# Optimization experiments

Hardware: AMD Instinct MI355X
Metric: run time of the kernel (lower is better)

The kernel has to match this reference:

```python
import jax, jax.numpy as jnp
import numpy as np

NUM_CATEGORIES = 32
INPUT_DIM = 1536
HIDDEN_DIM = 1024
OUTPUT_DIM = 1024
B, T = 128, 32


def setup_inputs() -> dict:
    key = jax.random.key(0)
    k_x, k_cat, k_w1, k_w2 = jax.random.split(key, 4)
    x = jax.random.normal(k_x, (B, T, INPUT_DIM), dtype=jnp.float32)
    cat_ids = jax.random.randint(k_cat, (B,), 0, NUM_CATEGORIES)
    # CategorySpecificLinear params: W ~ 0.02*randn, b = zeros
    W1 = 0.02 * jax.random.normal(k_w1, (NUM_CATEGORIES, INPUT_DIM, HIDDEN_DIM), dtype=jnp.float32)
    b1 = jnp.zeros((NUM_CATEGORIES, HIDDEN_DIM), dtype=jnp.float32)
    W2 = 0.02 * jax.random.normal(k_w2, (NUM_CATEGORIES, HIDDEN_DIM, OUTPUT_DIM), dtype=jnp.float32)
    b2 = jnp.zeros((NUM_CATEGORIES, OUTPUT_DIM), dtype=jnp.float32)
    return {"x": x, "cat_ids": cat_ids, "W1": W1, "b1": b1, "W2": W2, "b2": b2}


def _cat_linear(x, W, b, cat_ids):
    # x: (B, T, D_in); W: (C, D_in, D_out); b: (C, D_out)
    # torch: bmm(x, W[cat_ids]) + b[cat_ids].unsqueeze(1)
    return jnp.einsum("btd,bdh->bth", x, W[cat_ids]) + b[cat_ids][:, None, :]


def reference(x, cat_ids, W1, b1, W2, b2):
    # CategorySpecificMLP.forward
    hidden = jax.nn.relu(_cat_linear(x, W1, b1, cat_ids))  # (B, T, H)
    return _cat_linear(hidden, W2, b2, cat_ids)            # (B, T, O)
```

## Files before the change

kernel.cpp:

```cpp
#include <hip/hip_runtime.h>
#include <hip/hip_bf16.h>
#include <stdint.h>

#define NCAT 32
#define DIN  1536
#define DMID 1024
#define NB   128
#define TT   32

#define BM 128
#define BN 64
#define BK 32
#define LDA 40
#define MAXG 56
#define NTILE 16

typedef __attribute__((ext_vector_type(8))) short short8;
typedef __attribute__((ext_vector_type(4))) float f32x4;

static __device__ __forceinline__ unsigned int pk2bf(float lo, float hi) {
  unsigned short a = __builtin_bit_cast(unsigned short, __float2bfloat16(lo));
  unsigned short b = __builtin_bit_cast(unsigned short, __float2bfloat16(hi));
  return ((unsigned int)b << 16) | (unsigned int)a;
}

__global__ void build_groups(const int* __restrict__ cat_ids, int* __restrict__ wsi) {
  __shared__ int cats[NB];
  __shared__ int cnt[NCAT];
  __shared__ int off[NCAT];
  int t = threadIdx.x;
  cats[t] = cat_ids[t];
  __syncthreads();
  if (t < NCAT) {
    int n = 0;
    for (int b = 0; b < NB; b++) n += (cats[b] == t);
    cnt[t] = n;
  }
  __syncthreads();
  if (t == 0) {
    int acc = 0;
    for (int c = 0; c < NCAT; c++) { off[c] = acc; acc += cnt[c]; }
  }
  __syncthreads();
  if (t < NCAT) {
    int o = off[t];
    for (int b = 0; b < NB; b++)
      if (cats[b] == t) wsi[o++] = b;
  }
  if (t == 0) {
    int g = 0;
    for (int c = 0; c < NCAT; c++) {
      int n = cnt[c], o = off[c];
      for (int j = 0; j < n; j += 4) {
        wsi[132 + g * 4 + 0] = c;
        wsi[132 + g * 4 + 1] = o + j;
        wsi[132 + g * 4 + 2] = (n - j) < 4 ? (n - j) : 4;
        g++;
      }
    }
    wsi[128] = g;
  }
}

__global__ void cvt_x_bf16(const float* __restrict__ in, unsigned short* __restrict__ out) {
  int i = blockIdx.x * 256 + threadIdx.x;
  const float4* p = (const float4*)in + (size_t)i * 2;
  float4 a = p[0], b = p[1];
  ((uint4*)out)[i] = make_uint4(pk2bf(a.x, a.y), pk2bf(a.z, a.w),
                                pk2bf(b.x, b.y), pk2bf(b.z, b.w));
}

template <int LAYER>
__global__ __launch_bounds__(256)
void mlp_gemm(const unsigned short* __restrict__ A, const float* __restrict__ W,
              const float* __restrict__ bias, const int* __restrict__ wsi,
              void* __restrict__ Out, int K) {
  const int id = blockIdx.x;
  const int g  = (id & 7) + 8 * (id >> 7);
  const int t  = (id >> 3) & 15;
  if (g >= wsi[128]) return;
  const int cat   = wsi[132 + g * 4 + 0];
  const int start = wsi[132 + g * 4 + 1];
  const int cnt   = wsi[132 + g * 4 + 2];
  const int n0    = t * BN;

  __shared__ unsigned short As[2][BM * LDA];
  __shared__ unsigned short Bs[2][4 * BN * 8];

  const int tid  = threadIdx.x;
  const int lane = tid & 63;
  const int w    = tid >> 6;

  const int arow  = tid >> 1;
  const int khalf = (tid & 1) * 16;
  const int lb    = arow >> 5;
  const int tok   = arow & 31;
  const int lbc   = lb < (cnt - 1) ? lb : (cnt - 1);
  const int batch = wsi[start + lbc];
  const long grow = (long)(batch * TT + tok);
  const unsigned short* Arow = A + grow * (long)K + khalf;

  const float* Wcol = W + (size_t)cat * (size_t)K * 1024 + n0 + lane;

  f32x4 acc[4][2];
#pragma unroll
  for (int i = 0; i < 4; i++)
#pragma unroll
    for (int j = 0; j < 2; j++) acc[i][j] = (f32x4){0.f, 0.f, 0.f, 0.f};

  const int wm  = (w >> 1) * 64;
  const int wn  = (w & 1) * 32;
  const int kg  = lane >> 4;
  const int c16 = lane & 15;

  uint4 a0, a1;
  float br[8];
  auto load_tile = [&](int k0) {
    const uint4* ap = (const uint4*)(Arow + k0);
    a0 = ap[0];
    a1 = ap[1];
    const float* bp = Wcol + (size_t)(k0 + w * 8) * 1024;
#pragma unroll
    for (int r = 0; r < 8; r++) br[r] = bp[(size_t)r * 1024];
  };
  auto store_tile = [&](int buf) {
    *(uint4*)&As[buf][arow * LDA + khalf]     = a0;
    *(uint4*)&As[buf][arow * LDA + khalf + 8] = a1;
    uint4 bw = make_uint4(pk2bf(br[0], br[1]), pk2bf(br[2], br[3]),
                          pk2bf(br[4], br[5]), pk2bf(br[6], br[7]));
    *(uint4*)&Bs[buf][(w * BN + lane) * 8] = bw;
  };

  load_tile(0);
  store_tile(0);
  int cur = 0;

  for (int k0 = 0; k0 < K; k0 += BK) {
    __syncthreads();
    const bool more = (k0 + BK) < K;
    if (more) load_tile(k0 + BK);

    short8 afrag[4], bfrag[2];
#pragma unroll
    for (int i = 0; i < 4; i++)
      afrag[i] = *(const short8*)&As[cur][(wm + i * 16 + c16) * LDA + kg * 8];
#pragma unroll
    for (int j = 0; j < 2; j++)
      bfrag[j] = *(const short8*)&Bs[cur][(kg * BN + wn + j * 16 + c16) * 8];
#pragma unroll
    for (int i = 0; i < 4; i++)
#pragma unroll
      for (int j = 0; j < 2; j++)
        acc[i][j] = __builtin_amdgcn_mfma_f32_16x16x32_bf16(afrag[i], bfrag[j], acc[i][j], 0, 0, 0);

    if (more) store_tile(cur ^ 1);
    cur ^= 1;
  }

  const int rquad = (lane >> 4) * 4;
#pragma unroll
  for (int i = 0; i < 4; i++) {
#pragma unroll
    for (int j = 0; j < 2; j++) {
      int gcol = n0 + wn + j * 16 + c16;
      float bb = bias[cat * 1024 + gcol];
#pragma unroll
      for (int r = 0; r < 4; r++) {
        int lrow = wm + i * 16 + rquad + r;
        int lb2 = lrow >> 5;
        if (lb2 < cnt) {
          int b2 = wsi[start + lb2];
          long orow = (long)(b2 * TT + (lrow & 31));
          float v = acc[i][j][r] + bb;
          if constexpr (LAYER == 1) {
            v = fmaxf(v, 0.f);
            ((unsigned short*)Out)[orow * DMID + gcol] =
                __builtin_bit_cast(unsigned short, __float2bfloat16(v));
          } else {
            ((float*)Out)[orow * 1024 + gcol] = v;
          }
        }
      }
    }
  }
}

extern "C" void kernel_launch(void* const* d_in, const int* in_sizes, int n_in,
                              void* d_out, int out_size, void* d_ws, size_t ws_size,
                              hipStream_t stream) {
  const float* x       = (const float*)d_in[0];
  const int*   cat_ids = (const int*)d_in[1];
  const float* W1      = (const float*)d_in[2];
  const float* b1      = (const float*)d_in[3];
  const float* W2      = (const float*)d_in[4];
  const float* b2      = (const float*)d_in[5];
  float* out = (float*)d_out;

  int* wsi = (int*)d_ws;
  unsigned short* xbf    = (unsigned short*)((char*)d_ws + 8192);
  unsigned short* hidden = (unsigned short*)((char*)d_ws + 8192 + 12582912);

  build_groups<<<dim3(1), dim3(128), 0, stream>>>(cat_ids, wsi);
  cvt_x_bf16<<<dim3(3072), dim3(256), 0, stream>>>(x, xbf);
  mlp_gemm<1><<<dim3(NTILE * MAXG), dim3(256), 0, stream>>>(
      xbf, W1, b1, wsi, (void*)hidden, DIN);
  mlp_gemm<2><<<dim3(NTILE * MAXG), dim3(256), 0, stream>>>(
      hidden, W2, b2, wsi, (void*)out, DMID);
}
```

Before: 446.7 us.

## Deepen global-load prefetch to four register stages with LDS-only barriers

Replaces the single-tile register prefetch with four rotating register stages, so global loads for A and W are issued three k-tiles ahead of their LDS store. The plain __syncthreads is replaced by a barrier that waits only on LDS counters, so outstanding global loads stay in flight across barriers. This aims to hide the latency of the strided fp32 weight loads. In exchange it uses more registers, which can lower occupancy, and the tail issues redundant clamped loads.

```diff
diff --git a/kernel.cpp b/kernel.cpp
--- a/kernel.cpp
+++ b/kernel.cpp
@@ -22,6 +22,11 @@
   unsigned short a = __builtin_bit_cast(unsigned short, __float2bfloat16(lo));
   unsigned short b = __builtin_bit_cast(unsigned short, __float2bfloat16(hi));
   return ((unsigned int)b << 16) | (unsigned int)a;
+}
+
+static __device__ __forceinline__ void pipe_barrier() {
+  __builtin_amdgcn_s_waitcnt(0xc07f);
+  __builtin_amdgcn_s_barrier();
 }
 
 __global__ void build_groups(const int* __restrict__ cat_ids, int* __restrict__ wsi) {
@@ -113,49 +118,61 @@
   const int kg  = lane >> 4;
   const int c16 = lane & 15;
 
-  uint4 a0, a1;
-  float br[8];
-  auto load_tile = [&](int k0) {
-    const uint4* ap = (const uint4*)(Arow + k0);
-    a0 = ap[0];
-    a1 = ap[1];
-    const float* bp = Wcol + (size_t)(k0 + w * 8) * 1024;
-#pragma unroll
-    for (int r = 0; r < 8; r++) br[r] = bp[(size_t)r * 1024];
-  };
-  auto store_tile = [&](int buf) {
-    *(uint4*)&As[buf][arow * LDA + khalf]     = a0;
-    *(uint4*)&As[buf][arow * LDA + khalf + 8] = a1;
-    uint4 bw = make_uint4(pk2bf(br[0], br[1]), pk2bf(br[2], br[3]),
-                          pk2bf(br[4], br[5]), pk2bf(br[6], br[7]));
-    *(uint4*)&Bs[buf][(w * BN + lane) * 8] = bw;
-  };
-
-  load_tile(0);
-  store_tile(0);
-  int cur = 0;
-
-  for (int k0 = 0; k0 < K; k0 += BK) {
-    __syncthreads();
-    const bool more = (k0 + BK) < K;
-    if (more) load_tile(k0 + BK);
-
-    short8 afrag[4], bfrag[2];
-#pragma unroll
-    for (int i = 0; i < 4; i++)
-      afrag[i] = *(const short8*)&As[cur][(wm + i * 16 + c16) * LDA + kg * 8];
-#pragma unroll
-    for (int j = 0; j < 2; j++)
-      bfrag[j] = *(const short8*)&Bs[cur][(kg * BN + wn + j * 16 + c16) * 8];
-#pragma unroll
-    for (int i = 0; i < 4; i++)
-#pragma unroll
-      for (int j = 0; j < 2; j++)
-        acc[i][j] = __builtin_amdgcn_mfma_f32_16x16x32_bf16(afrag[i], bfrag[j], acc[i][j], 0, 0, 0);
-
-    if (more) store_tile(cur ^ 1);
-    cur ^= 1;
-  }
+  const int NT = K / BK;
+
+  uint4 s0_a0, s0_a1, s1_a0, s1_a1, s2_a0, s2_a1, s3_a0, s3_a1;
+  float s0_b[8], s1_b[8], s2_b[8], s3_b[8];
+
+#define ISSUE(S, KT) do {                                                  \
+    int kk_ = (KT) < NT ? (KT) : (NT - 1);                                 \
+    const uint4* ap_ = (const uint4*)(Arow + kk_ * BK);                    \
+    S##_a0 = ap_[0]; S##_a1 = ap_[1];                                      \
+    const float* bp_ = Wcol + (size_t)(kk_ * BK + w * 8) * 1024;           \
+    _Pragma("unroll")                                                      \
+    for (int r_ = 0; r_ < 8; r_++) S##_b[r_] = bp_[(size_t)r_ * 1024];     \
+  } while (0)
+
+#define STORE(S, BUF) do {                                                 \
+    *(uint4*)&As[BUF][arow * LDA + khalf]     = S##_a0;                    \
+    *(uint4*)&As[BUF][arow * LDA + khalf + 8] = S##_a1;                    \
+    *(uint4*)&Bs[BUF][(w * BN + lane) * 8] = make_uint4(                   \
+        pk2bf(S##_b[0], S##_b[1]), pk2bf(S##_b[2], S##_b[3]),              \
+        pk2bf(S##_b[4], S##_b[5]), pk2bf(S##_b[6], S##_b[7]));             \
+  } while (0)
+
+#define CONSUME(BUF) do {                                                  \
+    short8 af_[4], bg_[2];                                                 \
+    _Pragma("unroll")                                                      \
+    for (int i_ = 0; i_ < 4; i_++)                                         \
+      af_[i_] = *(const short8*)&As[BUF][(wm + i_ * 16 + c16) * LDA + kg * 8]; \
+    _Pragma("unroll")                                                      \
+    for (int j_ = 0; j_ < 2; j_++)                                         \
+      bg_[j_] = *(const short8*)&Bs[BUF][(kg * BN + wn + j_ * 16 + c16) * 8];  \
+    _Pragma("unroll")                                                      \
+    for (int i_ = 0; i_ < 4; i_++)                                         \
+      _Pragma("unroll")                                                    \
+      for (int j_ = 0; j_ < 2; j_++)                                       \
+        acc[i_][j_] = __builtin_amdgcn_mfma_f32_16x16x32_bf16(             \
+            af_[i_], bg_[j_], acc[i_][j_], 0, 0, 0);                       \
+  } while (0)
+
+  ISSUE(s0, 0);
+  ISSUE(s1, 1);
+  ISSUE(s2, 2);
+  ISSUE(s3, 3);
+  STORE(s0, 0);
+  pipe_barrier();
+
+  for (int T = 0; T < NT; T += 4) {
+    ISSUE(s0, T + 4); CONSUME(0); STORE(s1, 1); pipe_barrier();
+    ISSUE(s1, T + 5); CONSUME(1); STORE(s2, 0); pipe_barrier();
+    ISSUE(s2, T + 6); CONSUME(0); STORE(s3, 1); pipe_barrier();
+    ISSUE(s3, T + 7); CONSUME(1); STORE(s0, 0); pipe_barrier();
+  }
+
+#undef ISSUE
+#undef STORE
+#undef CONSUME
 
   const int rquad = (lane >> 4) * 4;
 #pragma unroll
```

New measurement: 460.4 us. 3.1% more time.
